# Optimization experiments

Measured on AMD Instinct MI355X. Metric: run time of the kernel, lower is better.

Reference implementation:

```python
import jax, jax.numpy as jnp
import numpy as np

EPS = 1e-5
GROUPS = 32

def group_norm(x, w, b):
    B, C, H, W = x.shape
    g = GROUPS
    xr = x.reshape(B, g, C // g, H * W)
    mean = xr.mean(axis=(2, 3), keepdims=True)
    var = xr.var(axis=(2, 3), keepdims=True)
    h = ((xr - mean) / jnp.sqrt(var + EPS)).reshape(B, C, H, W)
    return h * w[None, :, None, None] + b[None, :, None, None]

def setup_inputs() -> dict:
    key = jax.random.key(0)
    ks = jax.random.split(key, 7)
    B, C, H, W = 8, 256, 64, 64
    d = C // 8  # 32
    x = jax.random.normal(ks[0], (B, C, H, W), dtype=jnp.float32)
    norm_w = 1.0 + 0.1 * jax.random.normal(ks[1], (C,), dtype=jnp.float32)
    norm_b = 0.1 * jax.random.normal(ks[2], (C,), dtype=jnp.float32)
    s = 1.0 / np.sqrt(C)
    Wq = jax.random.normal(ks[3], (d, C), dtype=jnp.float32) * s
    Wk = jax.random.normal(ks[4], (d, C), dtype=jnp.float32) * s
    Wv = jax.random.normal(ks[5], (C, C), dtype=jnp.float32) * s
    Wproj = jax.random.normal(ks[6], (C, C), dtype=jnp.float32) * s
    gamma = jnp.full((1,), 0.5, dtype=jnp.float32)  # torch init is 0; nonzero so attention path contributes
    return {"x": x, "norm_w": norm_w, "norm_b": norm_b, "Wq": Wq, "Wk": Wk,
            "Wv": Wv, "Wproj": Wproj, "gamma": gamma}

def reference(x, norm_w, norm_b, Wq, Wk, Wv, Wproj, gamma):
    B, C, H, W = x.shape
    N = H * W
    h = group_norm(x, norm_w, norm_b)           # (B,C,H,W)
    hf = h.reshape(B, C, N)                      # flatten spatial
    d = Wq.shape[0]
    q = jnp.einsum('dc,bcn->bnd', Wq, hf)        # (B,N,d)
    k = jnp.einsum('dc,bcn->bdn', Wk, hf)        # (B,d,N)
    v = jnp.einsum('oc,bcn->bno', Wv, hf)        # (B,N,C)
    scale = d ** (-0.5)
    attn = jax.nn.softmax(jnp.einsum('bnd,bdm->bnm', q, k) * scale, axis=-1)  # (B,N,N)
    out = jnp.einsum('bnm,bmo->bno', attn, v)    # (B,N,C)
    out = out.transpose(0, 2, 1).reshape(B, C, H, W)
    proj = jnp.einsum('oc,bchw->bohw', Wproj, out)
    return x + gamma[0] * proj
```

## Files before the change

kernel.cpp:

```cpp
#include <hip/hip_runtime.h>
#include <cstdint>


typedef __bf16 bf16x8 __attribute__((ext_vector_type(8)));
typedef float f32x4 __attribute__((ext_vector_type(4)));
typedef float f32x16 __attribute__((ext_vector_type(16)));
typedef unsigned int u32x4 __attribute__((ext_vector_type(4)));
typedef unsigned short u16x4 __attribute__((ext_vector_type(4)));
typedef unsigned short u16x8 __attribute__((ext_vector_type(8)));

#define DEVI __device__ __forceinline__

DEVI unsigned short f2bf(float f) {
    __bf16 h = (__bf16)f;
    return __builtin_bit_cast(unsigned short, h);
}
DEVI float bf2f(unsigned short u) {
    unsigned int x = ((unsigned int)u) << 16;
    return __builtin_bit_cast(float, x);
}

DEVI f32x4 mfma16(bf16x8 a, bf16x8 b, f32x4 c) {
    return __builtin_amdgcn_mfma_f32_16x16x32_bf16(a, b, c, 0, 0, 0);
}
DEVI f32x16 mfma32(bf16x8 a, bf16x8 b, f32x16 c) {
    return __builtin_amdgcn_mfma_f32_32x32x16_bf16(a, b, c, 0, 0, 0);
}

DEVI void glds16(const unsigned short* g, unsigned short* l) {
    const __attribute__((address_space(1))) unsigned int* gp =
        reinterpret_cast<const __attribute__((address_space(1))) unsigned int*>(
            reinterpret_cast<uintptr_t>(g));
    __attribute__((address_space(3))) unsigned int* lp =
        reinterpret_cast<__attribute__((address_space(3))) unsigned int*>(
            reinterpret_cast<uintptr_t>(l));
    __builtin_amdgcn_global_load_lds(gp, lp, 16, 0, 0);
}

DEVI void barrier_raw() {
    asm volatile("" ::: "memory");
    __builtin_amdgcn_s_barrier();
    asm volatile("" ::: "memory");
}
DEVI void wait_vm0() {
    __builtin_amdgcn_s_waitcnt(0x3F70);
}

#define QSCALE 0.2550663133f
#define MFIX   12.0f

__global__ __launch_bounds__(256) void k_pack(
        const float* __restrict__ wq, const float* __restrict__ wk,
        const float* __restrict__ wv, const float* __restrict__ wp,
        unsigned short* __restrict__ bqk, unsigned short* __restrict__ bv,
        unsigned short* __restrict__ bp) {
    int i = blockIdx.x * 256 + threadIdx.x;
    if (i < 8192)       bqk[i] = f2bf(wq[i] * QSCALE);
    else if (i < 16384) bqk[i] = f2bf(wk[i - 8192]);
    bv[i] = f2bf(wv[i]);
    bp[i] = f2bf(wp[i]);
}

__global__ __launch_bounds__(1024) void k_gnorm(
        const float* __restrict__ x, const float* __restrict__ gw,
        const float* __restrict__ gb, unsigned short* __restrict__ ht) {
    int bg = blockIdx.x;
    int b = bg >> 5, g = bg & 31;
    const float* xb = x + ((size_t)(b * 256 + g * 8)) * 4096;
    int t = threadIdx.x;
    float s1 = 0.f, s2 = 0.f;
    const f32x4* xv4 = (const f32x4*)xb;
    for (int i = t; i < 8192; i += 1024) {
        f32x4 v = xv4[i];
        #pragma unroll
        for (int j = 0; j < 4; j++) { s1 += v[j]; s2 += v[j] * v[j]; }
    }
    #pragma unroll
    for (int off = 1; off < 64; off <<= 1) {
        s1 += __shfl_xor(s1, off);
        s2 += __shfl_xor(s2, off);
    }
    __shared__ float red[34];
    int wv_ = t >> 6;
    if ((t & 63) == 0) { red[wv_ * 2] = s1; red[wv_ * 2 + 1] = s2; }
    __syncthreads();
    if (t == 0) {
        float a = 0.f, q = 0.f;
        #pragma unroll
        for (int i = 0; i < 16; i++) { a += red[i * 2]; q += red[i * 2 + 1]; }
        float mean = a * (1.f / 32768.f);
        float var = q * (1.f / 32768.f) - mean * mean;
        red[32] = mean; red[33] = rsqrtf(var + 1e-5f);
    }
    __syncthreads();
    float mean = red[32], rstd = red[33];
    float wv8[8], bv8[8];
    #pragma unroll
    for (int c = 0; c < 8; c++) { wv8[c] = gw[g * 8 + c] * rstd; bv8[c] = gb[g * 8 + c] - mean * rstd * gw[g * 8 + c]; }
    int n0 = t * 4;
    f32x4 cv[8];
    #pragma unroll
    for (int c = 0; c < 8; c++) cv[c] = *(const f32x4*)(xb + c * 4096 + n0);
    #pragma unroll
    for (int j = 0; j < 4; j++) {
        u16x8 pk;
        #pragma unroll
        for (int c = 0; c < 8; c++) pk[c] = f2bf(cv[c][j] * wv8[c] + bv8[c]);
        *(u16x8*)(&ht[((size_t)(b * 4096 + n0 + j)) * 256 + g * 8]) = pk;
    }
}

template <int EPI>
__global__ __launch_bounds__(256) void k_gemm(
        const unsigned short* __restrict__ A, const unsigned short* __restrict__ Bw,
        void* __restrict__ outp, const float* __restrict__ xres,
        const float* __restrict__ gamma, int ldout) {
    __shared__ unsigned short lA[128 * 72];
    __shared__ unsigned short lB[64 * 72];
    int t = threadIdx.x;
    int m0 = blockIdx.x * 128, n0 = blockIdx.y * 64;
    int w = t >> 6, lane = t & 63, l15 = lane & 15, quad = lane >> 4;
    f32x4 z4 = {0.f, 0.f, 0.f, 0.f};
    f32x4 acc[2][4];
    #pragma unroll
    for (int i = 0; i < 2; i++)
        #pragma unroll
        for (int j = 0; j < 4; j++) acc[i][j] = z4;

    for (int kb = 0; kb < 4; kb++) {
        #pragma unroll
        for (int i = 0; i < 4; i++) {
            int ch = i * 256 + t;
            int row = ch >> 3, col = (ch & 7) * 8;
            u32x4 v = *(const u32x4*)(A + (size_t)(m0 + row) * 256 + kb * 64 + col);
            *(u32x4*)(&lA[row * 72 + col]) = v;
        }
        #pragma unroll
        for (int i = 0; i < 2; i++) {
            int ch = i * 256 + t;
            int row = ch >> 3, col = (ch & 7) * 8;
            u32x4 v = *(const u32x4*)(Bw + (size_t)(n0 + row) * 256 + kb * 64 + col);
            *(u32x4*)(&lB[row * 72 + col]) = v;
        }
        __syncthreads();
        #pragma unroll
        for (int ks = 0; ks < 2; ks++) {
            bf16x8 af[2], bfr[4];
            #pragma unroll
            for (int fr = 0; fr < 2; fr++)
                af[fr] = *(const bf16x8*)(&lA[(w * 32 + fr * 16 + l15) * 72 + ks * 32 + quad * 8]);
            #pragma unroll
            for (int fn = 0; fn < 4; fn++)
                bfr[fn] = *(const bf16x8*)(&lB[(fn * 16 + l15) * 72 + ks * 32 + quad * 8]);
            #pragma unroll
            for (int fr = 0; fr < 2; fr++)
                #pragma unroll
                for (int fn = 0; fn < 4; fn++)
                    acc[fr][fn] = mfma16(af[fr], bfr[fn], acc[fr][fn]);
        }
        __syncthreads();
    }

    if (EPI == 0) {
        unsigned short* out = (unsigned short*)outp;
        #pragma unroll
        for (int fr = 0; fr < 2; fr++)
            #pragma unroll
            for (int fn = 0; fn < 4; fn++)
                #pragma unroll
                for (int r = 0; r < 4; r++) {
                    int m = m0 + w * 32 + fr * 16 + quad * 4 + r;
                    int n = n0 + fn * 16 + l15;
                    out[(size_t)m * ldout + n] = f2bf(acc[fr][fn][r]);
                }
    } else if (EPI == 1) {
        unsigned short* out = (unsigned short*)outp;
        int b = m0 >> 12, nb = (m0 & 4095) + w * 32;
        int swq = ((quad & 1) << 1) | (quad >> 1);
        #pragma unroll
        for (int fr = 0; fr < 2; fr++)
            #pragma unroll
            for (int fn = 0; fn < 4; fn++) {
                int o = n0 + fn * 16 + l15;
                int n = nb + fr * 16 + swq * 4;
                u16x4 pk;
                #pragma unroll
                for (int r = 0; r < 4; r++) pk[r] = f2bf(acc[fr][fn][r]);
                *(u16x4*)(&out[(((size_t)(b * 256 + o)) << 12) + n]) = pk;
            }
    } else {
        float* out = (float*)outp;
        float gm = gamma[0];
        int b = m0 >> 12, nb = (m0 & 4095) + w * 32;
        #pragma unroll
        for (int fr = 0; fr < 2; fr++)
            #pragma unroll
            for (int fn = 0; fn < 4; fn++) {
                int o = n0 + fn * 16 + l15;
                int n = nb + fr * 16 + quad * 4;
                size_t base = (((size_t)(b * 256 + o)) << 12) + n;
                f32x4 xv = *(const f32x4*)(xres + base);
                f32x4 ov;
                #pragma unroll
                for (int r = 0; r < 4; r++) ov[r] = xv[r] + gm * acc[fr][fn][r];
                *(f32x4*)(out + base) = ov;
            }
    }
}

__global__ __launch_bounds__(256, 2) void k_flash(
        const unsigned short* __restrict__ QK, const unsigned short* __restrict__ Vt,
        unsigned short* __restrict__ Oa) {
    __shared__ __align__(16) char smem[40960];
    int id = blockIdx.x;
    int b = id & 7;
    int r3 = id >> 3;
    int oh = r3 & 1, qblk = r3 >> 1;
    int t = threadIdx.x, w = t >> 6, ln = t & 63;
    int l31 = ln & 31, h = ln >> 5;
    int qh = w >> 1, kh = w & 1;
    int q0 = qblk * 128 + qh * 64;

    bf16x8 qb0[2], qb1[2];
    #pragma unroll
    for (int qt2 = 0; qt2 < 2; qt2++) {
        const unsigned short* qrow = QK + ((size_t)(b * 4096 + q0 + qt2 * 32 + l31)) * 64;
        qb0[qt2] = *(const bf16x8*)(qrow + h * 8);
        qb1[qt2] = *(const bf16x8*)(qrow + 16 + h * 8);
    }

    int cgK = (ln & 3) ^ ((ln >> 2) & 3) ^ ((ln >> 4) & 3);
    const unsigned short* gK = QK + ((size_t)(b * 4096 + w * 16 + (ln >> 2))) * 64 + 32 + cgK * 8;
    int vc8 = (ln & 7) ^ ((ln >> 3) & 7);
    const unsigned short* gV = Vt + (((size_t)(b * 256 + oh * 128 + w * 32 + (ln >> 3))) << 12) + vc8 * 8;

    unsigned short* lK0 = (unsigned short*)smem;
    unsigned short* lV0 = (unsigned short*)(smem + 4096);
    unsigned short* lK1 = (unsigned short*)(smem + 20480);
    unsigned short* lV1 = (unsigned short*)(smem + 24576);
    unsigned short* sK0 = lK0 + w * 512;
    unsigned short* sV0 = lV0 + w * 2048;
    unsigned short* sK1 = lK1 + w * 512;
    unsigned short* sV1 = lV1 + w * 2048;

    f32x16 z16;
    #pragma unroll
    for (int i = 0; i < 16; i++) z16[i] = 0.f;
    f32x16 minit;
    #pragma unroll
    for (int i = 0; i < 16; i++) minit[i] = -MFIX;
    f32x16 Oacc[2][4];
    #pragma unroll
    for (int qt2 = 0; qt2 < 2; qt2++)
        #pragma unroll
        for (int i = 0; i < 4; i++) Oacc[qt2][i] = z16;
    float lsum[2] = {0.f, 0.f};

    int gl = (l31 & 3) ^ ((l31 >> 2) & 3);
    const unsigned short* kf0p0 = lK0 + (kh * 32 + l31) * 32 + ((0 + h) ^ gl) * 8;
    const unsigned short* kf1p0 = lK0 + (kh * 32 + l31) * 32 + ((2 + h) ^ gl) * 8;
    const unsigned short* kf0p1 = lK1 + (kh * 32 + l31) * 32 + ((0 + h) ^ gl) * 8;
    const unsigned short* kf1p1 = lK1 + (kh * 32 + l31) * 32 + ((2 + h) ^ gl) * 8;
    int slotA = ((kh * 4 + 0 * 2 + h) ^ (ln & 7)) * 8;
    int slotB = ((kh * 4 + 1 * 2 + h) ^ (ln & 7)) * 8;

    auto stage = [&](int kn, unsigned short* sK, unsigned short* sV) {
        glds16(gK + (size_t)kn * 4096, sK);
        #pragma unroll
        for (int j = 0; j < 4; j++)
            glds16(gV + ((size_t)j * 8 << 12) + kn * 64, sV + j * 512);
    };

    auto compute = [&](const unsigned short* kf0p, const unsigned short* kf1p,
                       const unsigned short* lV) {
        bf16x8 kf0 = *(const bf16x8*)kf0p;
        bf16x8 kf1 = *(const bf16x8*)kf1p;
        bf16x8 pa[2][2];
        #pragma unroll
        for (int qt2 = 0; qt2 < 2; qt2++) {
            f32x16 St = mfma32(kf0, qb0[qt2], minit);
            St = mfma32(kf1, qb1[qt2], St);
            u16x8 p0u, p1u;
            float s = 0.f;
            #pragma unroll
            for (int j = 0; j < 8; j++) {
                float e0 = __builtin_amdgcn_exp2f(St[j]);
                float e1 = __builtin_amdgcn_exp2f(St[8 + j]);
                s += e0 + e1;
                p0u[j] = f2bf(e0);
                p1u[j] = f2bf(e1);
            }
            lsum[qt2] += s;
            pa[qt2][0] = __builtin_bit_cast(bf16x8, p0u);
            pa[qt2][1] = __builtin_bit_cast(bf16x8, p1u);
        }
        #pragma unroll
        for (int nt = 0; nt < 4; nt++) {
            bf16x8 vf = *(const bf16x8*)(lV + (nt * 32 + l31) * 64 + slotA);
            Oacc[0][nt] = mfma32(pa[0][0], vf, Oacc[0][nt]);
            Oacc[1][nt] = mfma32(pa[1][0], vf, Oacc[1][nt]);
        }
        #pragma unroll
        for (int nt = 0; nt < 4; nt++) {
            bf16x8 vf = *(const bf16x8*)(lV + (nt * 32 + l31) * 64 + slotB);
            Oacc[0][nt] = mfma32(pa[0][1], vf, Oacc[0][nt]);
            Oacc[1][nt] = mfma32(pa[1][1], vf, Oacc[1][nt]);
        }
    };

    stage(0, sK0, sV0);
    for (int kt = 0; kt < 64; kt += 2) {
        wait_vm0();
        barrier_raw();
        stage(kt + 1, sK1, sV1);
        compute(kf0p0, kf1p0, lV0);
        wait_vm0();
        barrier_raw();
        if (kt + 2 < 64) stage(kt + 2, sK0, sV0);
        compute(kf0p1, kf1p1, lV1);
    }
    #pragma unroll
    for (int qt2 = 0; qt2 < 2; qt2++) lsum[qt2] += __shfl_xor(lsum[qt2], 32);
    __syncthreads();

    float* sf = (float*)smem;
    int lbase = (kh ? 8192 : 8320) + qh * 64 + l31;
    sf[lbase] = lsum[0];
    sf[lbase + 32] = lsum[1];
    if (kh == 1) {
        #pragma unroll
        for (int qt2 = 0; qt2 < 2; qt2++)
            #pragma unroll
            for (int nt = 0; nt < 4; nt++)
                #pragma unroll
                for (int rg = 0; rg < 2; rg++) {
                    u16x8 pk;
                    #pragma unroll
                    for (int j = 0; j < 8; j++) pk[j] = f2bf(Oacc[qt2][nt][rg * 8 + j]);
                    *(u16x8*)(smem + qh * 16384 + qt2 * 8192 + nt * 2048 + rg * 1024 + ln * 16) = pk;
                }
    }
    __syncthreads();
    if (kh == 0) {
        #pragma unroll
        for (int qt2 = 0; qt2 < 2; qt2++) {
            float rl[16];
            #pragma unroll
            for (int r = 0; r < 16; r++) {
                int row = (r & 3) + 8 * (r >> 2) + 4 * h;
                float l = sf[8192 + qh * 64 + qt2 * 32 + row] +
                          sf[8320 + qh * 64 + qt2 * 32 + row];
                rl[r] = 1.f / l;
            }
            size_t rb = (size_t)(b * 4096 + qblk * 128 + qh * 64 + qt2 * 32);
            #pragma unroll
            for (int nt = 0; nt < 4; nt++)
                #pragma unroll
                for (int rg = 0; rg < 2; rg++) {
                    u16x8 pk = *(const u16x8*)(smem + qh * 16384 + qt2 * 8192 + nt * 2048 + rg * 1024 + ln * 16);
                    #pragma unroll
                    for (int j = 0; j < 8; j++) {
                        int r = rg * 8 + j;
                        float val = (Oacc[qt2][nt][r] + bf2f(pk[j])) * rl[r];
                        int row = (r & 3) + 8 * (r >> 2) + 4 * h;
                        Oa[(rb + row) * 256 + oh * 128 + nt * 32 + l31] = f2bf(val);
                    }
                }
        }
    }
}

extern "C" void kernel_launch(void* const* d_in, const int* in_sizes, int n_in,
                              void* d_out, int out_size, void* d_ws, size_t ws_size,
                              hipStream_t stream) {
    const float* x  = (const float*)d_in[0];
    const float* nw = (const float*)d_in[1];
    const float* nb = (const float*)d_in[2];
    const float* wq = (const float*)d_in[3];
    const float* wk = (const float*)d_in[4];
    const float* wv = (const float*)d_in[5];
    const float* wp = (const float*)d_in[6];
    const float* gm = (const float*)d_in[7];

    char* p = (char*)d_ws;
    unsigned short* ht  = (unsigned short*)p; p += (size_t)32768 * 256 * 2;
    unsigned short* qk  = (unsigned short*)p; p += (size_t)32768 * 64 * 2;
    unsigned short* vt  = (unsigned short*)p; p += (size_t)8 * 256 * 4096 * 2;
    unsigned short* oa  = (unsigned short*)p; p += (size_t)32768 * 256 * 2;
    unsigned short* bqk = (unsigned short*)p; p += 64 * 256 * 2;
    unsigned short* bv  = (unsigned short*)p; p += 256 * 256 * 2;
    unsigned short* bp  = (unsigned short*)p; p += 256 * 256 * 2;

    k_pack<<<dim3(256), dim3(256), 0, stream>>>(wq, wk, wv, wp, bqk, bv, bp);
    k_gnorm<<<dim3(256), dim3(1024), 0, stream>>>(x, nw, nb, ht);
    k_gemm<0><<<dim3(256, 1), dim3(256), 0, stream>>>(ht, bqk, (void*)qk, nullptr, nullptr, 64);
    k_gemm<1><<<dim3(256, 4), dim3(256), 0, stream>>>(ht, bv, (void*)vt, nullptr, nullptr, 0);
    k_flash<<<dim3(512), dim3(256), 0, stream>>>(qk, vt, oa);
    k_gemm<2><<<dim3(256, 4), dim3(256), 0, stream>>>(oa, bp, d_out, x, gm, 0);
}
```

Measured before the change: 232.0 us.

## Deepen flash attention pipeline to four LDS stages with software-pipelined QK/PV

The flash kernel moves from a double-buffered to a four-buffer LDS ring. It waits on partial vmcnt instead of draining all loads, and software-pipelines the QK^T/exp of one tile against the PV MFMAs of the previous tile. The GEMM kernels for V and the projection also remap block IDs so the four N-tiles of each M row land on the same XCD, which should improve L2 reuse of A. The extra LDS (80KB per block) may cut occupancy from two blocks per CU, and the paired pa registers raise register pressure.

```diff
diff --git a/kernel.cpp b/kernel.cpp
--- a/kernel.cpp
+++ b/kernel.cpp
@@ -42,9 +42,8 @@
     __builtin_amdgcn_s_barrier();
     asm volatile("" ::: "memory");
 }
-DEVI void wait_vm0() {
-    __builtin_amdgcn_s_waitcnt(0x3F70);
-}
+DEVI void wait_vm0() { __builtin_amdgcn_s_waitcnt(0x3F70); }
+DEVI void wait_vm5() { __builtin_amdgcn_s_waitcnt(0x3F75); }
 
 #define QSCALE 0.2550663133f
 #define MFIX   12.0f
@@ -118,7 +117,15 @@
     __shared__ unsigned short lA[128 * 72];
     __shared__ unsigned short lB[64 * 72];
     int t = threadIdx.x;
-    int m0 = blockIdx.x * 128, n0 = blockIdx.y * 64;
+    int m0, n0;
+    if (EPI == 0) {
+        m0 = blockIdx.x * 128; n0 = blockIdx.y * 64;
+    } else {
+        int id = blockIdx.x;
+        int xcd = id & 7, r = id >> 3;
+        n0 = (r & 3) * 64;
+        m0 = ((r >> 2) * 8 + xcd) * 128;
+    }
     int w = t >> 6, lane = t & 63, l15 = lane & 15, quad = lane >> 4;
     f32x4 z4 = {0.f, 0.f, 0.f, 0.f};
     f32x4 acc[2][4];
@@ -211,7 +218,7 @@
 __global__ __launch_bounds__(256, 2) void k_flash(
         const unsigned short* __restrict__ QK, const unsigned short* __restrict__ Vt,
         unsigned short* __restrict__ Oa) {
-    __shared__ __align__(16) char smem[40960];
+    __shared__ __align__(16) char smem[81920];
     int id = blockIdx.x;
     int b = id & 7;
     int r3 = id >> 3;
@@ -234,14 +241,22 @@
     int vc8 = (ln & 7) ^ ((ln >> 3) & 7);
     const unsigned short* gV = Vt + (((size_t)(b * 256 + oh * 128 + w * 32 + (ln >> 3))) << 12) + vc8 * 8;
 
-    unsigned short* lK0 = (unsigned short*)smem;
-    unsigned short* lV0 = (unsigned short*)(smem + 4096);
-    unsigned short* lK1 = (unsigned short*)(smem + 20480);
-    unsigned short* lV1 = (unsigned short*)(smem + 24576);
-    unsigned short* sK0 = lK0 + w * 512;
-    unsigned short* sV0 = lV0 + w * 2048;
-    unsigned short* sK1 = lK1 + w * 512;
-    unsigned short* sV1 = lV1 + w * 2048;
+    unsigned short* const Kb0 = (unsigned short*)(smem);
+    unsigned short* const Vb0 = (unsigned short*)(smem + 4096);
+    unsigned short* const Kb1 = (unsigned short*)(smem + 20480);
+    unsigned short* const Vb1 = (unsigned short*)(smem + 24576);
+    unsigned short* const Kb2 = (unsigned short*)(smem + 40960);
+    unsigned short* const Vb2 = (unsigned short*)(smem + 45056);
+    unsigned short* const Kb3 = (unsigned short*)(smem + 61440);
+    unsigned short* const Vb3 = (unsigned short*)(smem + 65536);
+    unsigned short* const sK0 = Kb0 + w * 512;
+    unsigned short* const sV0 = Vb0 + w * 2048;
+    unsigned short* const sK1 = Kb1 + w * 512;
+    unsigned short* const sV1 = Vb1 + w * 2048;
+    unsigned short* const sK2 = Kb2 + w * 512;
+    unsigned short* const sV2 = Vb2 + w * 2048;
+    unsigned short* const sK3 = Kb3 + w * 512;
+    unsigned short* const sV3 = Vb3 + w * 2048;
 
     f32x16 z16;
     #pragma unroll
@@ -257,25 +272,21 @@
     float lsum[2] = {0.f, 0.f};
 
     int gl = (l31 & 3) ^ ((l31 >> 2) & 3);
-    const unsigned short* kf0p0 = lK0 + (kh * 32 + l31) * 32 + ((0 + h) ^ gl) * 8;
-    const unsigned short* kf1p0 = lK0 + (kh * 32 + l31) * 32 + ((2 + h) ^ gl) * 8;
-    const unsigned short* kf0p1 = lK1 + (kh * 32 + l31) * 32 + ((0 + h) ^ gl) * 8;
-    const unsigned short* kf1p1 = lK1 + (kh * 32 + l31) * 32 + ((2 + h) ^ gl) * 8;
-    int slotA = ((kh * 4 + 0 * 2 + h) ^ (ln & 7)) * 8;
-    int slotB = ((kh * 4 + 1 * 2 + h) ^ (ln & 7)) * 8;
-
-    auto stage = [&](int kn, unsigned short* sK, unsigned short* sV) {
-        glds16(gK + (size_t)kn * 4096, sK);
+    const int koff0 = (kh * 32 + l31) * 32 + ((0 + h) ^ gl) * 8;
+    const int koff1 = (kh * 32 + l31) * 32 + ((2 + h) ^ gl) * 8;
+    const int slotA = ((kh * 4 + 0 * 2 + h) ^ (ln & 7)) * 8;
+    const int slotB = ((kh * 4 + 1 * 2 + h) ^ (ln & 7)) * 8;
+
+    auto stage = [&](int kn, unsigned short* sKd, unsigned short* sVd) {
+        glds16(gK + (size_t)kn * 4096, sKd);
         #pragma unroll
         for (int j = 0; j < 4; j++)
-            glds16(gV + ((size_t)j * 8 << 12) + kn * 64, sV + j * 512);
+            glds16(gV + ((size_t)j * 8 << 12) + kn * 64, sVd + j * 512);
     };
 
-    auto compute = [&](const unsigned short* kf0p, const unsigned short* kf1p,
-                       const unsigned short* lV) {
-        bf16x8 kf0 = *(const bf16x8*)kf0p;
-        bf16x8 kf1 = *(const bf16x8*)kf1p;
-        bf16x8 pa[2][2];
+    auto qkexp = [&](const unsigned short* bK, bf16x8 (&pa)[2][2]) {
+        bf16x8 kf0 = *(const bf16x8*)(bK + koff0);
+        bf16x8 kf1 = *(const bf16x8*)(bK + koff1);
         #pragma unroll
         for (int qt2 = 0; qt2 < 2; qt2++) {
             f32x16 St = mfma32(kf0, qb0[qt2], minit);
@@ -294,31 +305,62 @@
             pa[qt2][0] = __builtin_bit_cast(bf16x8, p0u);
             pa[qt2][1] = __builtin_bit_cast(bf16x8, p1u);
         }
+    };
+
+    auto pv = [&](const unsigned short* bV, bf16x8 (&pa)[2][2]) {
         #pragma unroll
         for (int nt = 0; nt < 4; nt++) {
-            bf16x8 vf = *(const bf16x8*)(lV + (nt * 32 + l31) * 64 + slotA);
+            bf16x8 vf = *(const bf16x8*)(bV + (nt * 32 + l31) * 64 + slotA);
             Oacc[0][nt] = mfma32(pa[0][0], vf, Oacc[0][nt]);
             Oacc[1][nt] = mfma32(pa[1][0], vf, Oacc[1][nt]);
         }
         #pragma unroll
         for (int nt = 0; nt < 4; nt++) {
-            bf16x8 vf = *(const bf16x8*)(lV + (nt * 32 + l31) * 64 + slotB);
+            bf16x8 vf = *(const bf16x8*)(bV + (nt * 32 + l31) * 64 + slotB);
             Oacc[0][nt] = mfma32(pa[0][1], vf, Oacc[0][nt]);
             Oacc[1][nt] = mfma32(pa[1][1], vf, Oacc[1][nt]);
         }
     };
 
+    bf16x8 paA[2][2], paB[2][2];
+
     stage(0, sK0, sV0);
-    for (int kt = 0; kt < 64; kt += 2) {
-        wait_vm0();
-        barrier_raw();
-        stage(kt + 1, sK1, sV1);
-        compute(kf0p0, kf1p0, lV0);
-        wait_vm0();
-        barrier_raw();
-        if (kt + 2 < 64) stage(kt + 2, sK0, sV0);
-        compute(kf0p1, kf1p1, lV1);
-    }
+    stage(1, sK1, sV1);
+
+    wait_vm5(); barrier_raw();
+    stage(2, sK2, sV2);
+    qkexp(Kb0, paA);
+    wait_vm5(); barrier_raw();
+    stage(3, sK3, sV3);
+    qkexp(Kb1, paB);
+    pv(Vb0, paA);
+
+    for (int kt = 2; kt < 62; kt += 4) {
+        wait_vm5(); barrier_raw();
+        stage(kt + 2, sK0, sV0);
+        qkexp(Kb2, paA);
+        pv(Vb1, paB);
+        wait_vm5(); barrier_raw();
+        stage(kt + 3, sK1, sV1);
+        qkexp(Kb3, paB);
+        pv(Vb2, paA);
+        wait_vm5(); barrier_raw();
+        stage(kt + 4, sK2, sV2);
+        qkexp(Kb0, paA);
+        pv(Vb3, paB);
+        wait_vm5(); barrier_raw();
+        stage(kt + 5, sK3, sV3);
+        qkexp(Kb1, paB);
+        pv(Vb0, paA);
+    }
+    wait_vm5(); barrier_raw();
+    qkexp(Kb2, paA);
+    pv(Vb1, paB);
+    wait_vm0(); barrier_raw();
+    qkexp(Kb3, paB);
+    pv(Vb2, paA);
+    pv(Vb3, paB);
+
     #pragma unroll
     for (int qt2 = 0; qt2 < 2; qt2++) lsum[qt2] += __shfl_xor(lsum[qt2], 32);
     __syncthreads();
@@ -394,7 +436,7 @@
     k_pack<<<dim3(256), dim3(256), 0, stream>>>(wq, wk, wv, wp, bqk, bv, bp);
     k_gnorm<<<dim3(256), dim3(1024), 0, stream>>>(x, nw, nb, ht);
     k_gemm<0><<<dim3(256, 1), dim3(256), 0, stream>>>(ht, bqk, (void*)qk, nullptr, nullptr, 64);
-    k_gemm<1><<<dim3(256, 4), dim3(256), 0, stream>>>(ht, bv, (void*)vt, nullptr, nullptr, 0);
+    k_gemm<1><<<dim3(1024), dim3(256), 0, stream>>>(ht, bv, (void*)vt, nullptr, nullptr, 0);
     k_flash<<<dim3(512), dim3(256), 0, stream>>>(qk, vt, oa);
-    k_gemm<2><<<dim3(256, 4), dim3(256), 0, stream>>>(oa, bp, d_out, x, gm, 0);
-}
+    k_gemm<2><<<dim3(1024), dim3(256), 0, stream>>>(oa, bp, d_out, x, gm, 0);
+}
```

Result: slower. 543.0 us (+134.0%).

## Merge QK and V projection GEMMs into one launch; interleave softmax exp with PV MFMAs

Applied to the files above, without the earlier changes.

Combines the Q/K projection GEMM and the V projection GEMM into a single launch, with grid.y=5 selecting the weight source and epilogue. This removes one kernel launch and the tail between the two GEMMs. In the flash kernel it restructures the inner step so the exponentials for the second query tile are computed while the first tile's PV MFMAs issue, and raises wave priority around that region. The aim is to overlap transcendental ALU work with matrix-core work, at the cost of higher register pressure.

```diff
diff --git a/kernel.cpp b/kernel.cpp
--- a/kernel.cpp
+++ b/kernel.cpp
@@ -114,11 +114,17 @@
 __global__ __launch_bounds__(256) void k_gemm(
         const unsigned short* __restrict__ A, const unsigned short* __restrict__ Bw,
         void* __restrict__ outp, const float* __restrict__ xres,
-        const float* __restrict__ gamma, int ldout) {
+        const float* __restrict__ gamma, int ldout,
+        const unsigned short* __restrict__ Bw2, void* __restrict__ outp2) {
     __shared__ unsigned short lA[128 * 72];
     __shared__ unsigned short lB[64 * 72];
     int t = threadIdx.x;
     int m0 = blockIdx.x * 128, n0 = blockIdx.y * 64;
+    const unsigned short* Bsrc = Bw;
+    if (EPI == 3) {
+        if (blockIdx.y == 0) { n0 = 0; }
+        else { Bsrc = Bw2; n0 = (blockIdx.y - 1) * 64; }
+    }
     int w = t >> 6, lane = t & 63, l15 = lane & 15, quad = lane >> 4;
     f32x4 z4 = {0.f, 0.f, 0.f, 0.f};
     f32x4 acc[2][4];
@@ -139,7 +145,7 @@
         for (int i = 0; i < 2; i++) {
             int ch = i * 256 + t;
             int row = ch >> 3, col = (ch & 7) * 8;
-            u32x4 v = *(const u32x4*)(Bw + (size_t)(n0 + row) * 256 + kb * 64 + col);
+            u32x4 v = *(const u32x4*)(Bsrc + (size_t)(n0 + row) * 256 + kb * 64 + col);
             *(u32x4*)(&lB[row * 72 + col]) = v;
         }
         __syncthreads();
@@ -161,7 +167,9 @@
         __syncthreads();
     }
 
-    if (EPI == 0) {
+    bool epi0 = (EPI == 0) || (EPI == 3 && blockIdx.y == 0);
+    bool epi1 = (EPI == 1) || (EPI == 3 && blockIdx.y != 0);
+    if (epi0) {
         unsigned short* out = (unsigned short*)outp;
         #pragma unroll
         for (int fr = 0; fr < 2; fr++)
@@ -173,8 +181,8 @@
                     int n = n0 + fn * 16 + l15;
                     out[(size_t)m * ldout + n] = f2bf(acc[fr][fn][r]);
                 }
-    } else if (EPI == 1) {
-        unsigned short* out = (unsigned short*)outp;
+    } else if (epi1) {
+        unsigned short* out = (unsigned short*)((EPI == 3) ? outp2 : outp);
         int b = m0 >> 12, nb = (m0 & 4095) + w * 32;
         int swq = ((quad & 1) << 1) | (quad >> 1);
         #pragma unroll
@@ -275,37 +283,60 @@
                        const unsigned short* lV) {
         bf16x8 kf0 = *(const bf16x8*)kf0p;
         bf16x8 kf1 = *(const bf16x8*)kf1p;
-        bf16x8 pa[2][2];
-        #pragma unroll
-        for (int qt2 = 0; qt2 < 2; qt2++) {
-            f32x16 St = mfma32(kf0, qb0[qt2], minit);
-            St = mfma32(kf1, qb1[qt2], St);
-            u16x8 p0u, p1u;
-            float s = 0.f;
-            #pragma unroll
-            for (int j = 0; j < 8; j++) {
-                float e0 = __builtin_amdgcn_exp2f(St[j]);
-                float e1 = __builtin_amdgcn_exp2f(St[8 + j]);
-                s += e0 + e1;
-                p0u[j] = f2bf(e0);
-                p1u[j] = f2bf(e1);
-            }
-            lsum[qt2] += s;
-            pa[qt2][0] = __builtin_bit_cast(bf16x8, p0u);
-            pa[qt2][1] = __builtin_bit_cast(bf16x8, p1u);
-        }
+        f32x16 St0 = mfma32(kf0, qb0[0], minit);
+        St0 = mfma32(kf1, qb1[0], St0);
+        f32x16 St1 = mfma32(kf0, qb0[1], minit);
+        St1 = mfma32(kf1, qb1[1], St1);
+        u16x8 p00, p01;
+        float s0 = 0.f;
+        #pragma unroll
+        for (int j = 0; j < 8; j++) {
+            float e0 = __builtin_amdgcn_exp2f(St0[j]);
+            float e1 = __builtin_amdgcn_exp2f(St0[8 + j]);
+            s0 += e0 + e1;
+            p00[j] = f2bf(e0);
+            p01[j] = f2bf(e1);
+        }
+        lsum[0] += s0;
+        bf16x8 pa00 = __builtin_bit_cast(bf16x8, p00);
+        bf16x8 pa01 = __builtin_bit_cast(bf16x8, p01);
+        u16x8 p10, p11;
+        float s1 = 0.f;
+        __builtin_amdgcn_s_setprio(1);
         #pragma unroll
         for (int nt = 0; nt < 4; nt++) {
             bf16x8 vf = *(const bf16x8*)(lV + (nt * 32 + l31) * 64 + slotA);
-            Oacc[0][nt] = mfma32(pa[0][0], vf, Oacc[0][nt]);
-            Oacc[1][nt] = mfma32(pa[1][0], vf, Oacc[1][nt]);
+            Oacc[0][nt] = mfma32(pa00, vf, Oacc[0][nt]);
+            float e0 = __builtin_amdgcn_exp2f(St1[nt]);
+            float e1 = __builtin_amdgcn_exp2f(St1[8 + nt]);
+            s1 += e0 + e1;
+            p10[nt] = f2bf(e0);
+            p11[nt] = f2bf(e1);
         }
         #pragma unroll
         for (int nt = 0; nt < 4; nt++) {
             bf16x8 vf = *(const bf16x8*)(lV + (nt * 32 + l31) * 64 + slotB);
-            Oacc[0][nt] = mfma32(pa[0][1], vf, Oacc[0][nt]);
-            Oacc[1][nt] = mfma32(pa[1][1], vf, Oacc[1][nt]);
-        }
+            Oacc[0][nt] = mfma32(pa01, vf, Oacc[0][nt]);
+            float e0 = __builtin_amdgcn_exp2f(St1[4 + nt]);
+            float e1 = __builtin_amdgcn_exp2f(St1[12 + nt]);
+            s1 += e0 + e1;
+            p10[4 + nt] = f2bf(e0);
+            p11[4 + nt] = f2bf(e1);
+        }
+        lsum[1] += s1;
+        bf16x8 pa10 = __builtin_bit_cast(bf16x8, p10);
+        bf16x8 pa11 = __builtin_bit_cast(bf16x8, p11);
+        #pragma unroll
+        for (int nt = 0; nt < 4; nt++) {
+            bf16x8 vf = *(const bf16x8*)(lV + (nt * 32 + l31) * 64 + slotA);
+            Oacc[1][nt] = mfma32(pa10, vf, Oacc[1][nt]);
+        }
+        #pragma unroll
+        for (int nt = 0; nt < 4; nt++) {
+            bf16x8 vf = *(const bf16x8*)(lV + (nt * 32 + l31) * 64 + slotB);
+            Oacc[1][nt] = mfma32(pa11, vf, Oacc[1][nt]);
+        }
+        __builtin_amdgcn_s_setprio(0);
     };
 
     stage(0, sK0, sV0);
@@ -393,8 +424,7 @@
 
     k_pack<<<dim3(256), dim3(256), 0, stream>>>(wq, wk, wv, wp, bqk, bv, bp);
     k_gnorm<<<dim3(256), dim3(1024), 0, stream>>>(x, nw, nb, ht);
-    k_gemm<0><<<dim3(256, 1), dim3(256), 0, stream>>>(ht, bqk, (void*)qk, nullptr, nullptr, 64);
-    k_gemm<1><<<dim3(256, 4), dim3(256), 0, stream>>>(ht, bv, (void*)vt, nullptr, nullptr, 0);
+    k_gemm<3><<<dim3(256, 5), dim3(256), 0, stream>>>(ht, bqk, (void*)qk, nullptr, nullptr, 64, bv, (void*)vt);
     k_flash<<<dim3(512), dim3(256), 0, stream>>>(qk, vt, oa);
-    k_gemm<2><<<dim3(256, 4), dim3(256), 0, stream>>>(oa, bp, d_out, x, gm, 0);
-}
+    k_gemm<2><<<dim3(256, 4), dim3(256), 0, stream>>>(oa, bp, d_out, x, gm, 0, nullptr, nullptr);
+}
```

Result: slower. 269.0 us (+15.9%).
